# Optimization experiments

Hardware: AMD Instinct MI355X
Metric: run time of the kernel (lower is better)

The kernel has to match this reference:

```python
import jax, jax.numpy as jnp
import numpy as np

MAX_RADIUS = 0.9
TEMP = 0.1

def _to_poincare(x, W, b):
    # Linear + Tanh, then rescale into Poincare ball of radius 0.9
    h = jnp.tanh(x @ W.T + b)
    norm = jnp.clip(jnp.linalg.norm(h, axis=-1, keepdims=True), 1e-8, None)
    scale = jnp.where(norm > MAX_RADIUS, MAX_RADIUS / norm, jnp.ones_like(norm))
    return h * scale

def setup_inputs() -> dict:
    key = jax.random.key(0)
    kq, kw, kb, km, ko = jax.random.split(key, 5)
    B, N, D = 2048, 100000, 128
    return {
        "query": jax.random.normal(kq, (B, D), dtype=jnp.float32),
        "W": jax.random.normal(kw, (D, D), dtype=jnp.float32) * (1.0 / np.sqrt(D)),
        "b": jax.random.normal(kb, (D,), dtype=jnp.float32) * 0.01,
        "mem_emb": jax.random.normal(km, (N, D), dtype=jnp.float32),
        "mem_out": jax.random.normal(ko, (N, D), dtype=jnp.float32),
        "k": 16,
    }

def reference(query, W, b, mem_emb, mem_out, k):
    q = _to_poincare(query, W, b)          # [B, D]
    m = _to_poincare(mem_emb, W, b)        # [N, D]
    # Euclidean cdist via the GEMM form: ||q||^2 + ||m||^2 - 2 q.m
    q2 = jnp.sum(q * q, axis=-1, keepdims=True)           # [B, 1]
    m2 = jnp.sum(m * m, axis=-1)                          # [N]
    d2 = q2 + m2[None, :] - 2.0 * (q @ m.T)               # [B, N]
    dists = jnp.sqrt(jnp.maximum(d2, 1e-12))
    # k smallest distances
    neg_top, top_idx = jax.lax.top_k(-dists, k)           # [B, k]
    top_dists = -neg_top
    weights = jax.nn.softmax(-top_dists / TEMP, axis=-1)  # [B, k]
    outcomes = mem_out[top_idx]                           # [B, k, D]
    return weights, outcomes
```

## Files before the change

### kernel.cpp

```cpp
#include <hip/hip_runtime.h>
#include <hip/hip_bf16.h>
#include <math.h>

#define DIM 128
#define QB 128
#define MB 64
#define NSPLIT 32
#define KSEL 16
#define KOWN 4
#define RESCORE 32
#define IDXMASK 0x1FFFu
#define KEYMASK 0xFFFFE000u
#define M2MAX 3200

using bf16x8 = __attribute__((ext_vector_type(8))) short;
using f32x4  = __attribute__((ext_vector_type(4))) float;

__device__ inline unsigned short f2bf(float f) {
  __hip_bfloat16 h = __float2bfloat16(f);
  return __builtin_bit_cast(unsigned short, h);
}
__device__ inline unsigned uminu(unsigned a, unsigned b) {
  return __builtin_elementwise_min(a, b);
}
__device__ inline unsigned umaxu(unsigned a, unsigned b) {
  return __builtin_elementwise_max(a, b);
}
__device__ inline unsigned long long umin64(unsigned long long a,
                                            unsigned long long b) {
  return __builtin_elementwise_min(a, b);
}

__device__ inline f32x4 mfma16(bf16x8 a, bf16x8 b, f32x4 c) {
  return __builtin_amdgcn_mfma_f32_16x16x32_bf16(a, b, c, 0, 0, 0);
}

__device__ inline void gload_lds16(const void* g, void* l) {
  __builtin_amdgcn_global_load_lds(
      (const __attribute__((address_space(1))) void*)g,
      (__attribute__((address_space(3))) void*)l, 16, 0, 0);
}

__device__ inline void ins4(unsigned (&ks)[KOWN], unsigned c) {
  #pragma unroll
  for (int i = 0; i < KOWN; ++i) {
    const unsigned lo = uminu(c, ks[i]);
    c = umaxu(c, ks[i]);
    ks[i] = lo;
  }
}

__global__ __launch_bounds__(512) void poincare2_k(
    const float* __restrict__ Xm, int Rm,
    const float* __restrict__ Xq, int Rq,
    const float* __restrict__ W, const float* __restrict__ bias,
    float* __restrict__ Pm, float* __restrict__ Pm2,
    float* __restrict__ Pm2s, int npadm,
    unsigned short* __restrict__ Pmbf,
    float* __restrict__ Pq, float* __restrict__ Pq2, int nbm)
{
  __shared__ float Wl[DIM * DIM];
  __shared__ float nrm[128 * 17];
  __shared__ float norm2l[128];

  const int t  = threadIdx.x;
  const int cg = t & 15;
  const int rg = t >> 4;

  const bool ismem = (int)blockIdx.x < nbm;
  const float* X = ismem ? Xm : Xq;
  const int    R = ismem ? Rm : Rq;
  float*       P  = ismem ? Pm  : Pq;
  float*       P2 = ismem ? Pm2 : Pq2;
  unsigned short* Pbf = ismem ? Pmbf : nullptr;
  const int rbase = (ismem ? blockIdx.x : (blockIdx.x - nbm)) * 128;

  for (int i = t; i < DIM * 32; i += 512) {
    const int j = i >> 5, c = i & 31;
    const float4 v = *(const float4*)&W[j * DIM + c * 4];
    *(float4*)&Wl[j * DIM + ((c ^ ((j >> 3) & 7)) << 2)] = v;
  }
  float bj[8];
  #pragma unroll
  for (int u = 0; u < 8; ++u) bj[u] = bias[cg * 8 + u];

  const float* xr[4];
  #pragma unroll
  for (int v = 0; v < 4; ++v) {
    int row = rbase + rg + 32 * v;
    if (row > R - 1) row = R - 1;
    xr[v] = X + (size_t)row * DIM;
  }
  __syncthreads();

  float acc[4][8];
  #pragma unroll
  for (int v = 0; v < 4; ++v)
    #pragma unroll
    for (int u = 0; u < 8; ++u) acc[v][u] = bj[u];

  #pragma unroll 2
  for (int k4 = 0; k4 < 32; ++k4) {
    float4 xv[4], wv[8];
    #pragma unroll
    for (int v = 0; v < 4; ++v) xv[v] = *(const float4*)&xr[v][k4 * 4];
    #pragma unroll
    for (int u = 0; u < 8; ++u) {
      const int j = cg * 8 + u;
      wv[u] = *(const float4*)&Wl[j * DIM + ((k4 ^ ((j >> 3) & 7)) << 2)];
    }
    #pragma unroll
    for (int v = 0; v < 4; ++v)
      #pragma unroll
      for (int u = 0; u < 8; ++u) {
        acc[v][u] = fmaf(xv[v].x, wv[u].x, acc[v][u]);
        acc[v][u] = fmaf(xv[v].y, wv[u].y, acc[v][u]);
        acc[v][u] = fmaf(xv[v].z, wv[u].z, acc[v][u]);
        acc[v][u] = fmaf(xv[v].w, wv[u].w, acc[v][u]);
      }
  }

  #pragma unroll
  for (int v = 0; v < 4; ++v) {
    float pn = 0.f;
    #pragma unroll
    for (int u = 0; u < 8; ++u) {
      const float th = tanhf(acc[v][u]);
      acc[v][u] = th;
      pn = fmaf(th, th, pn);
    }
    nrm[(rg + 32 * v) * 17 + cg] = pn;
  }
  __syncthreads();
  if (t < 128) {
    float s = 0.f;
    #pragma unroll
    for (int c2 = 0; c2 < 16; ++c2) s += nrm[t * 17 + c2];
    norm2l[t] = s;
    const int row = rbase + t;
    if (row < R) {
      const float nm = sqrtf(s);
      const float sc = (nm > 0.9f) ? (0.9f / nm) : 1.0f;
      const float p2v = s * sc * sc;
      P2[row] = p2v;
      if (ismem) Pm2s[row] = fmaf(0.5f, p2v, 1.0f);
    } else if (ismem && row < npadm) {
      Pm2s[row] = __int_as_float(0x7f800000);
    }
  }
  __syncthreads();

  #pragma unroll
  for (int v = 0; v < 4; ++v) {
    const int r = rg + 32 * v;
    const int row = rbase + r;
    if (row < R) {
      const float n2 = norm2l[r];
      const float nm = sqrtf(n2);
      const float sc = (nm > 0.9f) ? (0.9f / nm) : 1.0f;
      float o[8];
      #pragma unroll
      for (int u = 0; u < 8; ++u) o[u] = acc[v][u] * sc;
      *(float4*)&P[(size_t)row * DIM + cg * 8]     = make_float4(o[0], o[1], o[2], o[3]);
      *(float4*)&P[(size_t)row * DIM + cg * 8 + 4] = make_float4(o[4], o[5], o[6], o[7]);
      if (Pbf) {
        uint4 pb;
        pb.x = (unsigned)f2bf(o[0]) | ((unsigned)f2bf(o[1]) << 16);
        pb.y = (unsigned)f2bf(o[2]) | ((unsigned)f2bf(o[3]) << 16);
        pb.z = (unsigned)f2bf(o[4]) | ((unsigned)f2bf(o[5]) << 16);
        pb.w = (unsigned)f2bf(o[6]) | ((unsigned)f2bf(o[7]) << 16);
        *(uint4*)&Pmbf[(size_t)row * DIM + ((cg ^ (row & 15)) << 3)] = pb;
      }
    }
  }
}

template<bool USEBF>
__global__ __launch_bounds__(512, 4) void score_topk_k(
    const float* __restrict__ Pq,
    const float* __restrict__ Pm, const float* __restrict__ Pm2s,
    const unsigned short* __restrict__ Pmbf,
    int N, int splitlen, unsigned* __restrict__ splitTop)
{
  __shared__ __align__(16) unsigned short Ml[3][MB * DIM];
  __shared__ float m2all[M2MAX];

  const int t = threadIdx.x;
  const int lane = t & 63;
  const int w = t >> 6, wr = w >> 1, wc = w & 1;
  const int split = blockIdx.x;
  const int qbase = blockIdx.y * QB;
  const int mlo = split * splitlen;
  const int mhi = min(mlo + splitlen, N);
  const int ntiles = (mhi - mlo + MB - 1) / MB;

  bf16x8 qf[2][4];
  #pragma unroll
  for (int s = 0; s < 2; ++s) {
    const int qrow = qbase + wr * 32 + s * 16 + (lane & 15);
    #pragma unroll
    for (int ks = 0; ks < 4; ++ks) {
      const float* src = &Pq[(size_t)qrow * DIM + ks * 32 + (lane >> 4) * 8];
      float4 lo = *(const float4*)src;
      float4 hi = *(const float4*)(src + 4);
      bf16x8 v;
      v[0] = (short)f2bf(-lo.x); v[1] = (short)f2bf(-lo.y);
      v[2] = (short)f2bf(-lo.z); v[3] = (short)f2bf(-lo.w);
      v[4] = (short)f2bf(-hi.x); v[5] = (short)f2bf(-hi.y);
      v[6] = (short)f2bf(-hi.z); v[7] = (short)f2bf(-hi.w);
      qf[s][ks] = v;
    }
  }

  for (int i = t; i < splitlen; i += 512) m2all[i] = Pm2s[mlo + i];

  const size_t soff0 = (size_t)(w * 8 + (lane >> 4)) * DIM + ((lane & 15) << 3);
  const size_t soff1 = soff0 + 4 * DIM;

  auto stageU = [&](int tilei, int buf) {
    const unsigned short* b = Pmbf + (size_t)(mlo + tilei * MB) * DIM;
    gload_lds16(b + soff0, &Ml[buf][(w * 8) * DIM]);
    gload_lds16(b + soff1, &Ml[buf][(w * 8 + 4) * DIM]);
  };
  uint4 sv0, sv1;
  auto stageF_load = [&](int tilei) {
    const int fr = t >> 3, fe = t & 7;
    const float* src = Pm + (size_t)(mlo + tilei * MB + fr) * DIM + fe * 16;
    float4 a0 = *(const float4*)(src + 0);
    float4 a1 = *(const float4*)(src + 4);
    float4 a2 = *(const float4*)(src + 8);
    float4 a3 = *(const float4*)(src + 12);
    sv0.x = (unsigned)f2bf(a0.x) | ((unsigned)f2bf(a0.y) << 16);
    sv0.y = (unsigned)f2bf(a0.z) | ((unsigned)f2bf(a0.w) << 16);
    sv0.z = (unsigned)f2bf(a1.x) | ((unsigned)f2bf(a1.y) << 16);
    sv0.w = (unsigned)f2bf(a1.z) | ((unsigned)f2bf(a1.w) << 16);
    sv1.x = (unsigned)f2bf(a2.x) | ((unsigned)f2bf(a2.y) << 16);
    sv1.y = (unsigned)f2bf(a2.z) | ((unsigned)f2bf(a2.w) << 16);
    sv1.z = (unsigned)f2bf(a3.x) | ((unsigned)f2bf(a3.y) << 16);
    sv1.w = (unsigned)f2bf(a3.z) | ((unsigned)f2bf(a3.w) << 16);
  };
  auto stageF_write = [&](int buf) {
    const int fr = t >> 3, fe = t & 7;
    char* base = (char*)&Ml[buf][0] + fr * 256;
    *(uint4*)(base + (((2 * fe)     ^ (fr & 15)) << 4)) = sv0;
    *(uint4*)(base + (((2 * fe + 1) ^ (fr & 15)) << 4)) = sv1;
  };

  unsigned keys[2][4][KOWN];
  #pragma unroll
  for (int s = 0; s < 2; ++s)
    #pragma unroll
    for (int r = 0; r < 4; ++r)
      #pragma unroll
      for (int i = 0; i < KOWN; ++i) keys[s][r][i] = 0xFFFFFFFFu;

  const int mcol = wc * 32 + (lane & 15);
  const int rowA = mcol, rowB = mcol + 16;

  auto compute = [&](int tile, const unsigned short* cur) {
    const float ca = m2all[tile * MB + mcol];
    const float cb = m2all[tile * MB + mcol + 16];
    f32x4 a00 = (f32x4){ca, ca, ca, ca};
    f32x4 a01 = (f32x4){cb, cb, cb, cb};
    f32x4 a10 = (f32x4){ca, ca, ca, ca};
    f32x4 a11 = (f32x4){cb, cb, cb, cb};
    __builtin_amdgcn_s_setprio(1);
    #pragma unroll
    for (int ks = 0; ks < 4; ++ks) {
      const int kb = ks * 64 + (lane >> 4) * 16;
      bf16x8 bfrA = *(const bf16x8*)((const char*)cur + rowA * 256 +
                                     (kb ^ ((rowA & 15) << 4)));
      bf16x8 bfrB = *(const bf16x8*)((const char*)cur + rowB * 256 +
                                     (kb ^ ((rowB & 15) << 4)));
      a00 = mfma16(qf[0][ks], bfrA, a00);
      a01 = mfma16(qf[0][ks], bfrB, a01);
      a10 = mfma16(qf[1][ks], bfrA, a10);
      a11 = mfma16(qf[1][ks], bfrB, a11);
    }
    __builtin_amdgcn_s_setprio(0);
    const unsigned idx0 = (unsigned)(tile * MB + mcol);
    #pragma unroll
    for (int r = 0; r < 4; ++r) {
      ins4(keys[0][r], (__float_as_uint(a00[r]) & KEYMASK) | idx0);
      ins4(keys[0][r], (__float_as_uint(a01[r]) & KEYMASK) | (idx0 + 16));
      ins4(keys[1][r], (__float_as_uint(a10[r]) & KEYMASK) | idx0);
      ins4(keys[1][r], (__float_as_uint(a11[r]) & KEYMASK) | (idx0 + 16));
    }
  };

  if constexpr (USEBF) {
    __syncthreads();
    stageU(0, 0);
    if (ntiles > 1) stageU(1, 1);
    int cur = 0;
    for (int i = 0; i < ntiles; ++i) {
      if (i < ntiles - 1) asm volatile("s_waitcnt vmcnt(2)" ::: "memory");
      else                asm volatile("s_waitcnt vmcnt(0)" ::: "memory");
      __builtin_amdgcn_s_barrier();
      __builtin_amdgcn_sched_barrier(0);
      int nb = cur + 2; if (nb >= 3) nb -= 3;
      if (i + 2 < ntiles) stageU(i + 2, nb);
      compute(i, &Ml[cur][0]);
      cur = (cur + 1 == 3) ? 0 : cur + 1;
    }
  } else {
    stageF_load(0);
    stageF_write(0);
    __syncthreads();
    for (int i = 0; i < ntiles; ++i) {
      const int cur = i & 1;
      const bool more = (i + 1 < ntiles);
      if (more) stageF_load(i + 1);
      compute(i, &Ml[cur][0]);
      __syncthreads();
      if (more) stageF_write(cur ^ 1);
      __syncthreads();
    }
  }

  #pragma unroll
  for (int s = 0; s < 2; ++s)
    #pragma unroll
    for (int r = 0; r < 4; ++r) {
      unsigned k0 = keys[s][r][0], k1 = keys[s][r][1];
      unsigned k2 = keys[s][r][2], k3 = keys[s][r][3];
      unsigned out = 0xFFFFFFFFu;
      for (int round = 0; round < 8; ++round) {
        unsigned g = k0;
        g = uminu(g, __shfl_xor(g, 1, 16));
        g = uminu(g, __shfl_xor(g, 2, 16));
        g = uminu(g, __shfl_xor(g, 4, 16));
        g = uminu(g, __shfl_xor(g, 8, 16));
        const bool mine = (k0 == g);
        k0 = mine ? k1 : k0;
        k1 = mine ? k2 : k1;
        k2 = mine ? k3 : k2;
        k3 = mine ? 0xFFFFFFFFu : k3;
        if ((lane & 15) == round) out = g;
      }
      const int q = qbase + wr * 32 + s * 16 + (lane >> 4) * 4 + r;
      if ((lane & 15) < 8)
        splitTop[(((size_t)q * NSPLIT + split) * 2 + wc) * 8 + (lane & 15)] = out;
    }
}

__global__ __launch_bounds__(256) void finalize_k(
    const unsigned* __restrict__ splitTop,
    const float* __restrict__ Pq, const float* __restrict__ Pq2,
    const float* __restrict__ Pm, const float* __restrict__ Pm2,
    const float* __restrict__ memOut, int N, int splitlen,
    float* __restrict__ outW, float* __restrict__ outO)
{
  const int wv   = threadIdx.x >> 6;
  const int lane = threadIdx.x & 63;
  const int q = blockIdx.x * 4 + wv;

  __shared__ unsigned      sKey[4][RESCORE];
  __shared__ unsigned char sSrc[4][RESCORE];
  __shared__ unsigned long long sKeyx[4][RESCORE];
  __shared__ unsigned long long sSel[4][KSEL];
  __shared__ float sEl[4][KSEL];

  {
    const unsigned* gp = splitTop + (size_t)q * (NSPLIT * 2 * 8) + lane * 8;
    unsigned a[8];
    uint4 lo = *(const uint4*)gp;
    uint4 hi = *(const uint4*)(gp + 4);
    a[0] = lo.x; a[1] = lo.y; a[2] = lo.z; a[3] = lo.w;
    a[4] = hi.x; a[5] = hi.y; a[6] = hi.z; a[7] = hi.w;
    for (int r = 0; r < RESCORE; ++r) {
      unsigned g = a[0];
      g = uminu(g, __shfl_xor(g, 1));
      g = uminu(g, __shfl_xor(g, 2));
      g = uminu(g, __shfl_xor(g, 4));
      g = uminu(g, __shfl_xor(g, 8));
      g = uminu(g, __shfl_xor(g, 16));
      g = uminu(g, __shfl_xor(g, 32));
      unsigned long long mask = __ballot(a[0] == g);
      const int fl = __ffsll((unsigned long long)mask) - 1;
      if (lane == fl) {
        #pragma unroll
        for (int i = 0; i < 7; ++i) a[i] = a[i + 1];
        a[7] = 0xFFFFFFFFu;
      }
      if (lane == 0) { sKey[wv][r] = g; sSrc[wv][r] = (unsigned char)fl; }
    }
  }

  #pragma unroll
  for (int p = 0; p < 4; ++p) {
    const int g8 = p * 8 + (lane >> 3), e = lane & 7;
    const int src = sSrc[wv][g8];
    const int gidx = (src >> 1) * splitlen + (int)(sKey[wv][g8] & IDXMASK);
    const float4* qr = (const float4*)&Pq[(size_t)q * DIM];
    const float4* mr = (const float4*)&Pm[(size_t)gidx * DIM];
    float s = 0.f;
    #pragma unroll
    for (int u = 0; u < 4; ++u) {
      float4 a = qr[e * 4 + u], b = mr[e * 4 + u];
      s = fmaf(a.x, b.x, s); s = fmaf(a.y, b.y, s);
      s = fmaf(a.z, b.z, s); s = fmaf(a.w, b.w, s);
    }
    s += __shfl_xor(s, 1, 8);
    s += __shfl_xor(s, 2, 8);
    s += __shfl_xor(s, 4, 8);
    if (e == 0) {
      float d2 = (Pq2[q] + Pm2[gidx]) - 2.0f * s;
      float dist = sqrtf(fmaxf(d2, 1e-12f));
      sKeyx[wv][g8] =
          (((unsigned long long)__float_as_uint(dist)) << 32) | (unsigned)gidx;
    }
  }

  {
    unsigned long long kk = (lane < RESCORE) ? sKeyx[wv][lane] : ~0ull;
    for (int r = 0; r < KSEL; ++r) {
      unsigned long long g = kk;
      g = umin64(g, __shfl_xor(g, 1));
      g = umin64(g, __shfl_xor(g, 2));
      g = umin64(g, __shfl_xor(g, 4));
      g = umin64(g, __shfl_xor(g, 8));
      g = umin64(g, __shfl_xor(g, 16));
      g = umin64(g, __shfl_xor(g, 32));
      if (kk == g) kk = ~0ull;
      if (lane == 0) sSel[wv][r] = g;
    }
  }

  if (lane < KSEL) {
    const float d  = __uint_as_float((unsigned)(sSel[wv][lane] >> 32));
    const float d0 = __uint_as_float((unsigned)(sSel[wv][0] >> 32));
    sEl[wv][lane] = expf((d0 - d) * 10.0f);
  }
  if (lane < KSEL) {
    float sum = 0.f;
    #pragma unroll
    for (int i = 0; i < KSEL; ++i) sum += sEl[wv][i];
    outW[(size_t)q * KSEL + lane] = sEl[wv][lane] / sum;
  }

  #pragma unroll
  for (int i = 0; i < 8; ++i) {
    const int f4 = lane + i * 64;
    const int r = f4 >> 5, c4 = f4 & 31;
    const int idx = (int)(sSel[wv][r] & 0xffffffffu);
    *(float4*)&outO[((size_t)q * KSEL + r) * DIM + c4 * 4] =
        *(const float4*)&memOut[(size_t)idx * DIM + c4 * 4];
  }
}

extern "C" void kernel_launch(void* const* d_in, const int* in_sizes, int n_in,
                              void* d_out, int out_size, void* d_ws, size_t ws_size,
                              hipStream_t stream)
{
  const float* query   = (const float*)d_in[0];
  const float* W       = (const float*)d_in[1];
  const float* bias    = (const float*)d_in[2];
  const float* mem_emb = (const float*)d_in[3];
  const float* mem_out = (const float*)d_in[4];
  const int B = in_sizes[0] / DIM;
  const int N = in_sizes[3] / DIM;

  const int splitlen = ((N + NSPLIT * MB - 1) / (NSPLIT * MB)) * MB;
  const int N_pad2 = NSPLIT * splitlen;

  float* ws  = (float*)d_ws;
  float* Pm  = ws;
  float* Pm2 = Pm + (size_t)N_pad2 * DIM;
  float* Pm2s = Pm2 + N_pad2;
  float* Pq  = Pm2s + N_pad2;
  float* Pq2 = Pq + (size_t)B * DIM;
  unsigned* splitTop = (unsigned*)(Pq2 + B);
  unsigned short* Pmbf = (unsigned short*)(splitTop + (size_t)B * NSPLIT * 2 * 8);
  const size_t need_bf = (size_t)((char*)(Pmbf + (size_t)N_pad2 * DIM) - (char*)d_ws);
  const bool usebf = ws_size >= need_bf;

  float* outW = (float*)d_out;
  float* outO = outW + (size_t)B * KSEL;

  const int nbm = (N_pad2 + 127) / 128;
  const int nbq = (B + 127) / 128;
  poincare2_k<<<dim3(nbm + nbq), dim3(512), 0, stream>>>(
      mem_emb, N, query, B, W, bias, Pm, Pm2, Pm2s, N_pad2,
      usebf ? Pmbf : nullptr, Pq, Pq2, nbm);

  dim3 grid2(NSPLIT, B / QB);
  if (usebf)
    score_topk_k<true><<<grid2, dim3(512), 0, stream>>>(Pq, Pm, Pm2s, Pmbf, N,
                                                        splitlen, splitTop);
  else
    score_topk_k<false><<<grid2, dim3(512), 0, stream>>>(Pq, Pm, Pm2s, nullptr, N,
                                                         splitlen, splitTop);

  finalize_k<<<dim3(B / 4), dim3(256), 0, stream>>>(splitTop, Pq, Pq2, Pm, Pm2,
                                                    mem_out, N, splitlen,
                                                    outW, outO);
}
```

Baseline: 211.6 us.

## Stream per-tile norms with LDS tiles, raise splits to 48 and occupancy

Removes the per-block LDS array holding all memory norms for a split and instead loads each tile's 64 norms alongside its bf16 tile via an async global-to-LDS load into the same triple buffer. This shrinks LDS per block so six blocks per CU can be resident. The split count goes from 32 to 48 to fill more CUs. The merge kernel is extended to take 96 partial lists per query using a second register queue. The trade-off is more partial candidates to merge, extra small loads per tile, and per-wave vmcnt bookkeeping.

Result: slower. 339.7 us (+60.6%).

```diff
diff --git a/kernel.cpp b/kernel.cpp
--- a/kernel.cpp
+++ b/kernel.cpp
@@ -5,13 +5,13 @@
 #define DIM 128
 #define QB 128
 #define MB 64
-#define NSPLIT 32
+#define NSPLIT 48
 #define KSEL 16
 #define KOWN 4
 #define RESCORE 32
 #define IDXMASK 0x1FFFu
 #define KEYMASK 0xFFFFE000u
-#define M2MAX 3200
+#define BUFB 16640
 
 using bf16x8 = __attribute__((ext_vector_type(8))) short;
 using f32x4  = __attribute__((ext_vector_type(4))) float;
@@ -39,6 +39,11 @@
   __builtin_amdgcn_global_load_lds(
       (const __attribute__((address_space(1))) void*)g,
       (__attribute__((address_space(3))) void*)l, 16, 0, 0);
+}
+__device__ inline void gload_lds4(const void* g, void* l) {
+  __builtin_amdgcn_global_load_lds(
+      (const __attribute__((address_space(1))) void*)g,
+      (__attribute__((address_space(3))) void*)l, 4, 0, 0);
 }
 
 __device__ inline void ins4(unsigned (&ks)[KOWN], unsigned c) {
@@ -176,14 +181,13 @@
 }
 
 template<bool USEBF>
-__global__ __launch_bounds__(512, 4) void score_topk_k(
+__global__ __launch_bounds__(512, 6) void score_topk_k(
     const float* __restrict__ Pq,
     const float* __restrict__ Pm, const float* __restrict__ Pm2s,
     const unsigned short* __restrict__ Pmbf,
     int N, int splitlen, unsigned* __restrict__ splitTop)
 {
-  __shared__ __align__(16) unsigned short Ml[3][MB * DIM];
-  __shared__ float m2all[M2MAX];
+  __shared__ __align__(16) char bufs[3][BUFB];
 
   const int t = threadIdx.x;
   const int lane = t & 63;
@@ -212,16 +216,18 @@
     }
   }
 
-  for (int i = t; i < splitlen; i += 512) m2all[i] = Pm2s[mlo + i];
-
   const size_t soff0 = (size_t)(w * 8 + (lane >> 4)) * DIM + ((lane & 15) << 3);
   const size_t soff1 = soff0 + 4 * DIM;
 
   auto stageU = [&](int tilei, int buf) {
-    const unsigned short* b = Pmbf + (size_t)(mlo + tilei * MB) * DIM;
-    gload_lds16(b + soff0, &Ml[buf][(w * 8) * DIM]);
-    gload_lds16(b + soff1, &Ml[buf][(w * 8 + 4) * DIM]);
+    const int mbase = mlo + tilei * MB;
+    const unsigned short* b = Pmbf + (size_t)mbase * DIM;
+    char* dst = bufs[buf];
+    gload_lds16(b + soff0, dst + (w * 8) * 256);
+    gload_lds16(b + soff1, dst + (w * 8 + 4) * 256);
+    if (w == 0) gload_lds4(Pm2s + mbase + lane, dst + 16384);
   };
+
   uint4 sv0, sv1;
   auto stageF_load = [&](int tilei) {
     const int fr = t >> 3, fe = t & 7;
@@ -239,11 +245,12 @@
     sv1.z = (unsigned)f2bf(a3.x) | ((unsigned)f2bf(a3.y) << 16);
     sv1.w = (unsigned)f2bf(a3.z) | ((unsigned)f2bf(a3.w) << 16);
   };
-  auto stageF_write = [&](int buf) {
+  auto stageF_write = [&](int tilei, int buf) {
     const int fr = t >> 3, fe = t & 7;
-    char* base = (char*)&Ml[buf][0] + fr * 256;
+    char* base = bufs[buf] + fr * 256;
     *(uint4*)(base + (((2 * fe)     ^ (fr & 15)) << 4)) = sv0;
     *(uint4*)(base + (((2 * fe + 1) ^ (fr & 15)) << 4)) = sv1;
+    if (t < MB) *(float*)(bufs[buf] + 16384 + 4 * t) = Pm2s[mlo + tilei * MB + t];
   };
 
   unsigned keys[2][4][KOWN];
@@ -257,9 +264,9 @@
   const int mcol = wc * 32 + (lane & 15);
   const int rowA = mcol, rowB = mcol + 16;
 
-  auto compute = [&](int tile, const unsigned short* cur) {
-    const float ca = m2all[tile * MB + mcol];
-    const float cb = m2all[tile * MB + mcol + 16];
+  auto compute = [&](int tile, const char* buf) {
+    const float ca = *(const float*)(buf + 16384 + 4 * mcol);
+    const float cb = *(const float*)(buf + 16384 + 4 * (mcol + 16));
     f32x4 a00 = (f32x4){ca, ca, ca, ca};
     f32x4 a01 = (f32x4){cb, cb, cb, cb};
     f32x4 a10 = (f32x4){ca, ca, ca, ca};
@@ -268,10 +275,8 @@
     #pragma unroll
     for (int ks = 0; ks < 4; ++ks) {
       const int kb = ks * 64 + (lane >> 4) * 16;
-      bf16x8 bfrA = *(const bf16x8*)((const char*)cur + rowA * 256 +
-                                     (kb ^ ((rowA & 15) << 4)));
-      bf16x8 bfrB = *(const bf16x8*)((const char*)cur + rowB * 256 +
-                                     (kb ^ ((rowB & 15) << 4)));
+      bf16x8 bfrA = *(const bf16x8*)(buf + rowA * 256 + (kb ^ ((rowA & 15) << 4)));
+      bf16x8 bfrB = *(const bf16x8*)(buf + rowB * 256 + (kb ^ ((rowB & 15) << 4)));
       a00 = mfma16(qf[0][ks], bfrA, a00);
       a01 = mfma16(qf[0][ks], bfrB, a01);
       a10 = mfma16(qf[1][ks], bfrA, a10);
@@ -289,31 +294,34 @@
   };
 
   if constexpr (USEBF) {
-    __syncthreads();
     stageU(0, 0);
     if (ntiles > 1) stageU(1, 1);
     int cur = 0;
     for (int i = 0; i < ntiles; ++i) {
-      if (i < ntiles - 1) asm volatile("s_waitcnt vmcnt(2)" ::: "memory");
-      else                asm volatile("s_waitcnt vmcnt(0)" ::: "memory");
+      if (i < ntiles - 1) {
+        if (w == 0) asm volatile("s_waitcnt vmcnt(3)" ::: "memory");
+        else        asm volatile("s_waitcnt vmcnt(2)" ::: "memory");
+      } else {
+        asm volatile("s_waitcnt vmcnt(0)" ::: "memory");
+      }
       __builtin_amdgcn_s_barrier();
       __builtin_amdgcn_sched_barrier(0);
       int nb = cur + 2; if (nb >= 3) nb -= 3;
       if (i + 2 < ntiles) stageU(i + 2, nb);
-      compute(i, &Ml[cur][0]);
+      compute(i, bufs[cur]);
       cur = (cur + 1 == 3) ? 0 : cur + 1;
     }
   } else {
     stageF_load(0);
-    stageF_write(0);
+    stageF_write(0, 0);
     __syncthreads();
     for (int i = 0; i < ntiles; ++i) {
       const int cur = i & 1;
       const bool more = (i + 1 < ntiles);
       if (more) stageF_load(i + 1);
-      compute(i, &Ml[cur][0]);
+      compute(i, bufs[cur]);
       __syncthreads();
-      if (more) stageF_write(cur ^ 1);
+      if (more) stageF_write(i + 1, cur ^ 1);
       __syncthreads();
     }
   }
@@ -363,27 +371,46 @@
 
   {
     const unsigned* gp = splitTop + (size_t)q * (NSPLIT * 2 * 8) + lane * 8;
-    unsigned a[8];
+    unsigned a[8], c[8];
     uint4 lo = *(const uint4*)gp;
     uint4 hi = *(const uint4*)(gp + 4);
     a[0] = lo.x; a[1] = lo.y; a[2] = lo.z; a[3] = lo.w;
     a[4] = hi.x; a[5] = hi.y; a[6] = hi.z; a[7] = hi.w;
+    if (lane < 32) {
+      const unsigned* gp2 = gp + 64 * 8;
+      uint4 lo2 = *(const uint4*)gp2;
+      uint4 hi2 = *(const uint4*)(gp2 + 4);
+      c[0] = lo2.x; c[1] = lo2.y; c[2] = lo2.z; c[3] = lo2.w;
+      c[4] = hi2.x; c[5] = hi2.y; c[6] = hi2.z; c[7] = hi2.w;
+    } else {
+      #pragma unroll
+      for (int i = 0; i < 8; ++i) c[i] = 0xFFFFFFFFu;
+    }
     for (int r = 0; r < RESCORE; ++r) {
-      unsigned g = a[0];
+      const unsigned myhead = uminu(a[0], c[0]);
+      unsigned g = myhead;
       g = uminu(g, __shfl_xor(g, 1));
       g = uminu(g, __shfl_xor(g, 2));
       g = uminu(g, __shfl_xor(g, 4));
       g = uminu(g, __shfl_xor(g, 8));
       g = uminu(g, __shfl_xor(g, 16));
       g = uminu(g, __shfl_xor(g, 32));
-      unsigned long long mask = __ballot(a[0] == g);
+      unsigned long long mask = __ballot(myhead == g);
       const int fl = __ffsll((unsigned long long)mask) - 1;
       if (lane == fl) {
-        #pragma unroll
-        for (int i = 0; i < 7; ++i) a[i] = a[i + 1];
-        a[7] = 0xFFFFFFFFu;
+        sKey[wv][r] = g;
+        if (a[0] == g) {
+          sSrc[wv][r] = (unsigned char)lane;
+          #pragma unroll
+          for (int i = 0; i < 7; ++i) a[i] = a[i + 1];
+          a[7] = 0xFFFFFFFFu;
+        } else {
+          sSrc[wv][r] = (unsigned char)(64 + lane);
+          #pragma unroll
+          for (int i = 0; i < 7; ++i) c[i] = c[i + 1];
+          c[7] = 0xFFFFFFFFu;
+        }
       }
-      if (lane == 0) { sKey[wv][r] = g; sSrc[wv][r] = (unsigned char)fl; }
     }
   }
 
```
